# Kernel optimization log

Measured on AMD Instinct MI355X. Metric: run time of the kernel, lower is better.

## Reference

```python
import jax, jax.numpy as jnp
import numpy as np

H, KV, D = 16, 4, 128
EPS = 1e-6

def setup_inputs() -> dict:
    key = jax.random.key(0)
    ks = jax.random.split(key, 7)
    B, S, HS = 2, 2048, 2048
    return {
        "hidden_states": jax.random.normal(ks[0], (B, S, HS), jnp.float32),
        "cos": jax.random.uniform(ks[1], (S, D), jnp.float32),
        "sin": jax.random.uniform(ks[2], (S, D), jnp.float32),
        "Wq": jax.random.normal(ks[3], (H * D, HS), jnp.float32) * 0.02,
        "Wk": jax.random.normal(ks[4], (KV * D, HS), jnp.float32) * 0.02,
        "Wv": jax.random.normal(ks[5], (KV * D, HS), jnp.float32) * 0.02,
        "Wo": jax.random.normal(ks[6], (HS, H * D), jnp.float32) * 0.02,
        "norm_q_w": jnp.ones((D,), jnp.float32),
        "norm_k_w": jnp.ones((D,), jnp.float32),
    }

def _rmsnorm(x, w):
    # RMSNorm over head_dim
    return x * jax.lax.rsqrt(jnp.mean(x * x, axis=-1, keepdims=True) + EPS) * w

def _rope(x, cos, sin):
    # x: [B, S, heads, D]; cos/sin: [S, D]; rotate-half (use_real_unbind_dim=-2)
    c = cos[None, :, None, :]
    s = sin[None, :, None, :]
    x1, x2 = jnp.split(x, 2, axis=-1)
    x_rot = jnp.concatenate([-x2, x1], axis=-1)
    return x * c + x_rot * s

def reference(hidden_states, cos, sin, Wq, Wk, Wv, Wo, norm_q_w, norm_k_w):
    B, S, _ = hidden_states.shape
    q = (hidden_states @ Wq.T).reshape(B, S, H, D)
    k = (hidden_states @ Wk.T).reshape(B, S, KV, D)
    v = (hidden_states @ Wv.T).reshape(B, S, KV, D)
    q = _rmsnorm(q, norm_q_w)
    k = _rmsnorm(k, norm_k_w)
    q = _rope(q, cos, sin)
    k = _rope(k, cos, sin)
    # GQA: repeat_interleave K/V heads to match Q heads
    g = H // KV
    k = jnp.repeat(k, g, axis=2)  # [B, S, H, D]
    v = jnp.repeat(v, g, axis=2)
    scores = jnp.einsum('bqhd,bkhd->bhqk', q, k) * (D ** -0.5)
    attn = jax.nn.softmax(scores, axis=-1)
    out = jnp.einsum('bhqk,bkhd->bqhd', attn, v)  # [B, S, H, D]
    out = out.reshape(B, S, H * D)
    return out @ Wo.T
```

## Files before the change

### kernel.cpp

```cpp
#include <hip/hip_runtime.h>


typedef __attribute__((ext_vector_type(8))) short bf16x8;
typedef __attribute__((ext_vector_type(4))) float f32x4;
typedef __attribute__((ext_vector_type(16))) float f32x16;

__device__ __forceinline__ unsigned short f2bf(float x) {
  union { float f; unsigned u; } v; v.f = x;
  unsigned r = v.u + 0x7fffu + ((v.u >> 16) & 1u);
  return (unsigned short)(r >> 16);
}

__device__ __forceinline__ unsigned cvt_pk_bf16(float lo, float hi) {
  unsigned r;
  asm("v_cvt_pk_bf16_f32 %0, %1, %2" : "=v"(r) : "v"(lo), "v"(hi));
  return r;
}

__device__ __forceinline__ void gload_lds16(const void* g, void* l) {
  __builtin_amdgcn_global_load_lds(
      (const __attribute__((address_space(1))) void*)g,
      (__attribute__((address_space(3))) void*)l, 16, 0, 0);
}

__global__ __launch_bounds__(256) void cvt4(const float4* __restrict__ in,
                                            ushort4* __restrict__ out, int n4) {
  int i = blockIdx.x * 256 + threadIdx.x;
  if (i < n4) {
    float4 v = in[i];
    out[i] = make_ushort4(f2bf(v.x), f2bf(v.y), f2bf(v.z), f2bf(v.w));
  }
}

__global__ __launch_bounds__(256) void gemm_bt_f32(
    const unsigned short* __restrict__ A, const unsigned short* __restrict__ B,
    float* __restrict__ C, int M, int N, int K) {
  __shared__ unsigned short lsA[128 * 32];
  __shared__ unsigned short lsB[128 * 32];
  const int tid = threadIdx.x;
  const int wave = tid >> 6;
  const int lane = tid & 63;
  const int lrow = lane & 15;
  const int kg = lane >> 4;
  const int nbn = N >> 7;
  const int bm = blockIdx.x / nbn;
  const int bn = blockIdx.x % nbn;
  const int m0 = bm << 7, n0 = bn << 7;
  const int wm = (wave >> 1) << 6, wn = (wave & 1) << 6;
  const f32x4 zero = {0.f, 0.f, 0.f, 0.f};
  f32x4 acc[4][4];
#pragma unroll
  for (int i = 0; i < 4; ++i)
#pragma unroll
    for (int j = 0; j < 4; ++j) acc[i][j] = zero;
  const int srow = tid >> 2;
  const int scol = (tid & 3) << 3;

  for (int k0 = 0; k0 < K; k0 += 32) {
    __syncthreads();
    gload_lds16(A + (size_t)(m0 + srow) * K + k0 + scol, (char*)lsA + wave * 1024);
    gload_lds16(A + (size_t)(m0 + 64 + srow) * K + k0 + scol, (char*)lsA + 4096 + wave * 1024);
    gload_lds16(B + (size_t)(n0 + srow) * K + k0 + scol, (char*)lsB + wave * 1024);
    gload_lds16(B + (size_t)(n0 + 64 + srow) * K + k0 + scol, (char*)lsB + 4096 + wave * 1024);
    __syncthreads();
    bf16x8 fa[4], fb[4];
#pragma unroll
    for (int i = 0; i < 4; ++i) {
      fa[i] = *(const bf16x8*)(lsA + ((wm + i * 16 + lrow) << 5) + (kg << 3));
      fb[i] = *(const bf16x8*)(lsB + ((wn + i * 16 + lrow) << 5) + (kg << 3));
    }
#pragma unroll
    for (int i = 0; i < 4; ++i)
#pragma unroll
      for (int j = 0; j < 4; ++j)
        acc[i][j] = __builtin_amdgcn_mfma_f32_16x16x32_bf16(fa[i], fb[j], acc[i][j], 0, 0, 0);
  }
#pragma unroll
  for (int i = 0; i < 4; ++i) {
#pragma unroll
    for (int j = 0; j < 4; ++j) {
      int col = n0 + wn + j * 16 + lrow;
      int rbase = m0 + wm + i * 16 + kg * 4;
#pragma unroll
      for (int t = 0; t < 4; ++t)
        C[(size_t)(rbase + t) * N + col] = acc[i][j][t];
    }
  }
}

__global__ __launch_bounds__(256) void rms_rope(
    const float* __restrict__ QKV, const float* __restrict__ cosT,
    const float* __restrict__ sinT, const float* __restrict__ wq,
    const float* __restrict__ wk, unsigned short* __restrict__ Q,
    unsigned short* __restrict__ Kg, unsigned short* __restrict__ Vg) {
  int task = blockIdx.x * 4 + (threadIdx.x >> 6);
  int lane = threadIdx.x & 63;
  int row = task / 24;
  int slot = task - row * 24;
  int b = row >> 11, s = row & 2047;
  const float* x = QKV + (size_t)row * 3072 + slot * 128;
  float x1 = x[lane], x2 = x[lane + 64];
  if (slot < 20) {
    float ss = x1 * x1 + x2 * x2;
#pragma unroll
    for (int msk = 1; msk < 64; msk <<= 1) ss += __shfl_xor(ss, msk);
    float inv = rsqrtf(ss * (1.0f / 128.0f) + 1e-6f);
    const float* w = (slot < 16) ? wq : wk;
    x1 *= inv * w[lane];
    x2 *= inv * w[lane + 64];
    float c1 = cosT[s * 128 + lane], c2 = cosT[s * 128 + lane + 64];
    float sn1 = sinT[s * 128 + lane], sn2 = sinT[s * 128 + lane + 64];
    float o1 = x1 * c1 - x2 * sn1;
    float o2 = x2 * c2 + x1 * sn2;
    if (slot < 16) {
      const float qs = 0.08838834764831845f * 1.4426950408889634f;
      o1 *= qs; o2 *= qs;
    }
    x1 = o1; x2 = o2;
  }
  if (slot < 16) {
    unsigned short* dst = Q + (((size_t)b * 16 + slot) * 2048 + s) * 128;
    dst[lane] = f2bf(x1);
    dst[lane + 64] = f2bf(x2);
  } else {
    int kv = (slot - 16) & 3;
    size_t tb = ((size_t)((b * 4 + kv) * 32) + (s >> 6)) * 16384;
    int key = s & 63;
    if (slot < 20) {
      char* base = (char*)Kg + tb;
      int xr = (key & 7) << 4;
      *(unsigned short*)(base + key * 256 + ((lane * 2) ^ xr)) = f2bf(x1);
      *(unsigned short*)(base + key * 256 + (((lane + 64) * 2) ^ xr)) = f2bf(x2);
    } else {
      char* base = (char*)Vg + tb;
      int p = key >> 4;
      int vhi = (key >> 2) & 1;
      int e = (key & 3) | (((key >> 3) & 1) << 2);
      int off = p * 4096 + vhi * 512 + e * 2;
      int d1 = lane, d2 = lane + 64;
      *(unsigned short*)(base + off + (d1 >> 5) * 1024 + (d1 & 31) * 16) = f2bf(x1);
      *(unsigned short*)(base + off + (d2 >> 5) * 1024 + (d2 & 31) * 16) = f2bf(x2);
    }
  }
}

__global__ __launch_bounds__(256, 2) void attn64(
    const unsigned short* __restrict__ Q, const unsigned short* __restrict__ Kg,
    const unsigned short* __restrict__ Vg, unsigned short* __restrict__ O) {
  __shared__ unsigned short Kl[2][8192];
  __shared__ unsigned short Vl[2][8192];
  const int tid = threadIdx.x;
  const int wave = tid >> 6, lane = tid & 63;
  const int l31 = lane & 31, hi = lane >> 5;
  int bid = blockIdx.x;
  bid = (bid & 7) * 64 + (bid >> 3);
  const int bh = bid >> 4, qt = bid & 15;
  const int b = bh >> 4, h = bh & 15, kh = h >> 2;
  const char* Kt = (const char*)Kg + (size_t)(b * 4 + kh) * 524288;
  const char* Vt = (const char*)Vg + (size_t)(b * 4 + kh) * 524288;
  const unsigned short* Qb =
      Q + ((size_t)(b * 16 + h) * 2048 + qt * 128 + wave * 32) * 128;
  bf16x8 qf[8];
#pragma unroll
  for (int s = 0; s < 8; ++s)
    qf[s] = *(const bf16x8*)(Qb + l31 * 128 + s * 16 + hi * 8);
  f32x16 acc[4];
#pragma unroll
  for (int c = 0; c < 4; ++c)
#pragma unroll
    for (int r = 0; r < 16; ++r) acc[c][r] = 0.f;
  float m = -1e30f, lsum = 0.f;
  const int xrk = (l31 & 7) << 4;

#pragma unroll
  for (int c = 0; c < 4; ++c) {
    gload_lds16(Kt + c * 4096 + tid * 16, (char*)Kl[0] + c * 4096 + wave * 1024);
    gload_lds16(Vt + c * 4096 + tid * 16, (char*)Vl[0] + c * 4096 + wave * 1024);
  }
  __syncthreads();

  for (int t = 0; t < 32; ++t) {
    const int cur = t & 1;
    if (t < 31) {
      const char* kt = Kt + (size_t)(t + 1) * 16384;
      const char* vt = Vt + (size_t)(t + 1) * 16384;
#pragma unroll
      for (int c = 0; c < 4; ++c) {
        gload_lds16(kt + c * 4096 + tid * 16, (char*)Kl[cur ^ 1] + c * 4096 + wave * 1024);
        gload_lds16(vt + c * 4096 + tid * 16, (char*)Vl[cur ^ 1] + c * 4096 + wave * 1024);
      }
    }
    const char* Kb = (const char*)Kl[cur];
    const char* Vb = (const char*)Vl[cur];
    f32x16 s0, s1;
#pragma unroll
    for (int r = 0; r < 16; ++r) { s0[r] = 0.f; s1[r] = 0.f; }
    __builtin_amdgcn_s_setprio(1);
#pragma unroll
    for (int s = 0; s < 8; ++s) {
      int xo = (s * 32 + hi * 16) ^ xrk;
      bf16x8 k0 = *(const bf16x8*)(Kb + l31 * 256 + xo);
      bf16x8 k1 = *(const bf16x8*)(Kb + (32 + l31) * 256 + xo);
      s0 = __builtin_amdgcn_mfma_f32_32x32x16_bf16(k0, qf[s], s0, 0, 0, 0);
      s1 = __builtin_amdgcn_mfma_f32_32x32x16_bf16(k1, qf[s], s1, 0, 0, 0);
    }
    __builtin_amdgcn_s_setprio(0);
    float t8[8];
#pragma unroll
    for (int r = 0; r < 8; ++r)
      t8[r] = fmaxf(fmaxf(s0[r], s0[r + 8]), fmaxf(s1[r], s1[r + 8]));
#pragma unroll
    for (int r = 0; r < 4; ++r) t8[r] = fmaxf(t8[r], t8[r + 4]);
    float mx = fmaxf(fmaxf(t8[0], t8[1]), fmaxf(t8[2], t8[3]));
    mx = fmaxf(mx, __shfl_xor(mx, 32));
    if (__any(mx > m + 8.f)) {
      float mn = fmaxf(m, mx);
      float sc = exp2f(m - mn);
      m = mn;
      lsum *= sc;
#pragma unroll
      for (int r = 0; r < 16; ++r) {
        float scq = __shfl(sc, (r & 3) + 8 * (r >> 2) + 4 * hi);
#pragma unroll
        for (int c = 0; c < 4; ++c) acc[c][r] *= scq;
      }
    }
    float p0[16], p1[16];
#pragma unroll
    for (int r = 0; r < 16; ++r) {
      p0[r] = exp2f(s0[r] - m);
      p1[r] = exp2f(s1[r] - m);
    }
    float u8[8];
#pragma unroll
    for (int r = 0; r < 8; ++r) u8[r] = (p0[r] + p0[r + 8]) + (p1[r] + p1[r + 8]);
#pragma unroll
    for (int r = 0; r < 4; ++r) u8[r] += u8[r + 4];
    float sum = (u8[0] + u8[1]) + (u8[2] + u8[3]);
    sum += __shfl_xor(sum, 32);
    lsum += sum;
    union { bf16x8 v[4]; unsigned w[16]; } pa;
#pragma unroll
    for (int r = 0; r < 4; ++r) {
      pa.w[r]      = cvt_pk_bf16(p0[2 * r], p0[2 * r + 1]);
      pa.w[4 + r]  = cvt_pk_bf16(p0[8 + 2 * r], p0[9 + 2 * r]);
      pa.w[8 + r]  = cvt_pk_bf16(p1[2 * r], p1[2 * r + 1]);
      pa.w[12 + r] = cvt_pk_bf16(p1[8 + 2 * r], p1[9 + 2 * r]);
    }
    __builtin_amdgcn_s_setprio(1);
#pragma unroll
    for (int p = 0; p < 4; ++p)
#pragma unroll
      for (int c = 0; c < 4; ++c) {
        bf16x8 vf = *(const bf16x8*)(Vb + p * 4096 + c * 1024 + hi * 512 + l31 * 16);
        acc[c] = __builtin_amdgcn_mfma_f32_32x32x16_bf16(pa.v[p], vf, acc[c], 0, 0, 0);
      }
    __builtin_amdgcn_s_setprio(0);
    __syncthreads();
  }
  float inv = 1.0f / lsum;
#pragma unroll
  for (int r = 0; r < 16; ++r) {
    int q = (r & 3) + 8 * (r >> 2) + 4 * hi;
    float invq = __shfl(inv, q);
    int srow = qt * 128 + wave * 32 + q;
    unsigned short* dst = O + (((size_t)b * 2048 + srow) * 16 + h) * 128;
#pragma unroll
    for (int c = 0; c < 4; ++c)
      dst[c * 32 + l31] = f2bf(acc[c][r] * invq);
  }
}

extern "C" void kernel_launch(void* const* d_in, const int* in_sizes, int n_in,
                              void* d_out, int out_size, void* d_ws, size_t ws_size,
                              hipStream_t stream) {
  const float* hs   = (const float*)d_in[0];
  const float* cosT = (const float*)d_in[1];
  const float* sinT = (const float*)d_in[2];
  const float* Wq   = (const float*)d_in[3];
  const float* Wk   = (const float*)d_in[4];
  const float* Wv   = (const float*)d_in[5];
  const float* Wo   = (const float*)d_in[6];
  const float* nqw  = (const float*)d_in[7];
  const float* nkw  = (const float*)d_in[8];
  float* out = (float*)d_out;

  char* ws = (char*)d_ws;
  unsigned short* X    = (unsigned short*)ws;
  unsigned short* Wqkv = X + 8388608;
  unsigned short* WoB  = Wqkv + 6291456;
  float* QKV           = (float*)(WoB + 4194304);
  unsigned short* Qb   = (unsigned short*)(QKV + 12582912);
  unsigned short* Kg   = Qb + 8388608;
  unsigned short* Vg   = Kg + 2097152;
  unsigned short* Ob   = (unsigned short*)QKV;

  cvt4<<<8192, 256, 0, stream>>>((const float4*)hs, (ushort4*)X, 2097152);
  cvt4<<<4096, 256, 0, stream>>>((const float4*)Wq, (ushort4*)Wqkv, 1048576);
  cvt4<<<1024, 256, 0, stream>>>((const float4*)Wk, (ushort4*)(Wqkv + 4194304), 262144);
  cvt4<<<1024, 256, 0, stream>>>((const float4*)Wv, (ushort4*)(Wqkv + 5242880), 262144);
  cvt4<<<4096, 256, 0, stream>>>((const float4*)Wo, (ushort4*)WoB, 1048576);

  gemm_bt_f32<<<32 * 24, 256, 0, stream>>>(X, Wqkv, QKV, 4096, 3072, 2048);

  rms_rope<<<24576, 256, 0, stream>>>(QKV, cosT, sinT, nqw, nkw, Qb, Kg, Vg);

  attn64<<<512, 256, 0, stream>>>(Qb, Kg, Vg, Ob);

  gemm_bt_f32<<<32 * 16, 256, 0, stream>>>(Ob, WoB, out, 4096, 2048, 2048);
}
```

Before: 260.5 us.

## Software-pipeline attention loop to issue next QK MFMAs alongside current PV

Restructures the flash-attention loop so that the QK^T MFMAs for tile t+1 are issued right after the softmax of tile t, interleaved with tile t's PV MFMAs. Two sets of score registers alternate between iterations, and the K/V prefetch is issued two tiles ahead after the barrier. The aim is to overlap the exp and max VALU work with matrix-core work and hide LDS latency. In exchange it raises register pressure and adds a barrier per iteration.

Result: no change. 260.9 us (+0.1%).

```diff
diff --git a/kernel.cpp b/kernel.cpp
--- a/kernel.cpp
+++ b/kernel.cpp
@@ -172,30 +172,22 @@
   float m = -1e30f, lsum = 0.f;
   const int xrk = (l31 & 7) << 4;
 
-#pragma unroll
-  for (int c = 0; c < 4; ++c) {
-    gload_lds16(Kt + c * 4096 + tid * 16, (char*)Kl[0] + c * 4096 + wave * 1024);
-    gload_lds16(Vt + c * 4096 + tid * 16, (char*)Vl[0] + c * 4096 + wave * 1024);
-  }
-  __syncthreads();
-
-  for (int t = 0; t < 32; ++t) {
-    const int cur = t & 1;
-    if (t < 31) {
-      const char* kt = Kt + (size_t)(t + 1) * 16384;
-      const char* vt = Vt + (size_t)(t + 1) * 16384;
-#pragma unroll
-      for (int c = 0; c < 4; ++c) {
-        gload_lds16(kt + c * 4096 + tid * 16, (char*)Kl[cur ^ 1] + c * 4096 + wave * 1024);
-        gload_lds16(vt + c * 4096 + tid * 16, (char*)Vl[cur ^ 1] + c * 4096 + wave * 1024);
-      }
-    }
-    const char* Kb = (const char*)Kl[cur];
-    const char* Vb = (const char*)Vl[cur];
-    f32x16 s0, s1;
+  auto stage = [&](int t) {
+    const char* kt = Kt + (size_t)t * 16384;
+    const char* vt = Vt + (size_t)t * 16384;
+    char* kd = (char*)Kl[t & 1];
+    char* vd = (char*)Vl[t & 1];
+#pragma unroll
+    for (int c = 0; c < 4; ++c) {
+      gload_lds16(kt + c * 4096 + tid * 16, kd + c * 4096 + wave * 1024);
+      gload_lds16(vt + c * 4096 + tid * 16, vd + c * 4096 + wave * 1024);
+    }
+  };
+
+  auto qk = [&](int t, f32x16& s0, f32x16& s1) {
+    const char* Kb = (const char*)Kl[t & 1];
 #pragma unroll
     for (int r = 0; r < 16; ++r) { s0[r] = 0.f; s1[r] = 0.f; }
-    __builtin_amdgcn_s_setprio(1);
 #pragma unroll
     for (int s = 0; s < 8; ++s) {
       int xo = (s * 32 + hi * 16) ^ xrk;
@@ -204,11 +196,13 @@
       s0 = __builtin_amdgcn_mfma_f32_32x32x16_bf16(k0, qf[s], s0, 0, 0, 0);
       s1 = __builtin_amdgcn_mfma_f32_32x32x16_bf16(k1, qf[s], s1, 0, 0, 0);
     }
-    __builtin_amdgcn_s_setprio(0);
+  };
+
+  auto body = [&](int t, f32x16& c0, f32x16& c1, f32x16& n0, f32x16& n1) {
     float t8[8];
 #pragma unroll
     for (int r = 0; r < 8; ++r)
-      t8[r] = fmaxf(fmaxf(s0[r], s0[r + 8]), fmaxf(s1[r], s1[r + 8]));
+      t8[r] = fmaxf(fmaxf(c0[r], c0[r + 8]), fmaxf(c1[r], c1[r + 8]));
 #pragma unroll
     for (int r = 0; r < 4; ++r) t8[r] = fmaxf(t8[r], t8[r + 4]);
     float mx = fmaxf(fmaxf(t8[0], t8[1]), fmaxf(t8[2], t8[3]));
@@ -228,8 +222,8 @@
     float p0[16], p1[16];
 #pragma unroll
     for (int r = 0; r < 16; ++r) {
-      p0[r] = exp2f(s0[r] - m);
-      p1[r] = exp2f(s1[r] - m);
+      p0[r] = exp2f(c0[r] - m);
+      p1[r] = exp2f(c1[r] - m);
     }
     float u8[8];
 #pragma unroll
@@ -247,7 +241,10 @@
       pa.w[8 + r]  = cvt_pk_bf16(p1[2 * r], p1[2 * r + 1]);
       pa.w[12 + r] = cvt_pk_bf16(p1[8 + 2 * r], p1[9 + 2 * r]);
     }
+    __syncthreads();
     __builtin_amdgcn_s_setprio(1);
+    if (t + 1 < 32) qk(t + 1, n0, n1);
+    const char* Vb = (const char*)Vl[t & 1];
 #pragma unroll
     for (int p = 0; p < 4; ++p)
 #pragma unroll
@@ -257,7 +254,20 @@
       }
     __builtin_amdgcn_s_setprio(0);
     __syncthreads();
-  }
+    if (t + 2 < 32) stage(t + 2);
+  };
+
+  stage(0);
+  __syncthreads();
+  f32x16 s0A, s1A, s0B, s1B;
+  qk(0, s0A, s1A);
+  stage(1);
+
+  for (int t = 0; t < 32; t += 2) {
+    body(t, s0A, s1A, s0B, s1B);
+    body(t + 1, s0B, s1B, s0A, s1A);
+  }
+
   float inv = 1.0f / lsum;
 #pragma unroll
   for (int r = 0; r < 16; ++r) {
```
